# Kernel optimization log

Measured on AMD Instinct MI355X. Metric: run time of the kernel, lower is better.

The kernel has to match this reference:

```python
import jax, jax.numpy as jnp
import numpy as np

N_NODES = 100000


def gcn_conv(x, src, dst, ew, W, b, n):
    """PyG GCNConv: self-loops (weight 1), symmetric norm, linear + bias.
    src/dst/ew already include self-loops."""
    xw = x @ W  # [N, out]
    deg = jax.ops.segment_sum(ew, dst, num_segments=n)  # in-degree with weights
    dinv = jnp.where(deg > 0, jax.lax.rsqrt(deg), 0.0)
    norm = dinv[src] * ew * dinv[dst]  # [E]
    msgs = xw[src] * norm[:, None]  # gather + scale
    out = jax.ops.segment_sum(msgs, dst, num_segments=n)  # scatter-add
    return out + b


def setup_inputs() -> dict:
    key = jax.random.key(0)
    k1, k2, k3, k4, k5 = jax.random.split(key, 5)
    x = jax.random.normal(k1, (N_NODES, 512), dtype=jnp.float32)
    edge_index = jax.random.randint(k2, (2, 3200000), 0, N_NODES, dtype=jnp.int64)
    edge_weight = jax.random.uniform(k3, (3200000,), dtype=jnp.float32)
    W1 = jax.random.normal(k4, (512, 64), dtype=jnp.float32) * (1.0 / np.sqrt(512))
    b1 = jnp.zeros((64,), dtype=jnp.float32)
    W2 = jax.random.normal(k5, (64, 20), dtype=jnp.float32) * (1.0 / np.sqrt(64))
    b2 = jnp.zeros((20,), dtype=jnp.float32)
    return {"x": x, "edge_index": edge_index, "edge_weight": edge_weight,
            "W1": W1, "b1": b1, "W2": W2, "b2": b2}


def reference(x, edge_index, edge_weight, W1, b1, W2, b2):
    n = x.shape[0]
    loops = jnp.arange(n, dtype=edge_index.dtype)
    src = jnp.concatenate([edge_index[0], loops])
    dst = jnp.concatenate([edge_index[1], loops])
    ew = jnp.concatenate([edge_weight, jnp.ones((n,), dtype=edge_weight.dtype)])
    h = gcn_conv(x, src, dst, ew, W1, b1, n)
    h = jax.nn.relu(h)  # dropout is identity in eval mode
    h = gcn_conv(h, src, dst, ew, W2, b2, n)
    return jax.nn.softmax(h, axis=-1)
```

## Files before the change

### kernel.cpp

```cpp
#include <hip/hip_runtime.h>
#include <hip/hip_fp16.h>
#include <math.h>

#define FIN 512
#define H   64
#define C   20
#define CP  32

typedef _Float16 half8 __attribute__((ext_vector_type(8)));
typedef float floatx4 __attribute__((ext_vector_type(4)));

__device__ __forceinline__ int detect_m64(const int* __restrict__ ei) {
    int nz = 0;
    #pragma unroll
    for (int i = 0; i < 32; i++) nz |= ei[2 * i + 1];
    return nz == 0;
}

__device__ __forceinline__ int edge_val(const int* __restrict__ ei, long long idx, int m64) {
    return m64 ? ei[2 * idx] : ei[(int)idx];
}

__global__ void init_kernel(const float* __restrict__ W, _Float16* __restrict__ W1T,
                            unsigned long long* __restrict__ packed, int N) {
    int tid = blockIdx.x * 256 + threadIdx.x;
    if (tid < H * FIN) {
        int n = tid >> 9, k = tid & 511;
        W1T[tid] = (_Float16)W[k * H + n];
    }
    if (tid < N) packed[tid] = 0ULL;
}

#define FIXSCALE 268435456.0f
#define KC 64
#define GM 64
#define HE 2048
__global__ __launch_bounds__(256, 8) void fused_gemm1_hist_kernel(
        const float* __restrict__ x, const _Float16* __restrict__ W1T,
        float* __restrict__ xw1f, int N,
        const int* __restrict__ ei, const float* __restrict__ ew,
        unsigned long long* __restrict__ packed, int* __restrict__ rankdst,
        int E, int GB, int HB) {
    __shared__ _Float16 xsh[GM][72];
    __shared__ _Float16 wsh[64][72];

    int nb = blockIdx.x;
    int minB = (GB < HB) ? GB : HB;
    int isHist, roleId;
    if (nb < 2 * minB) { isHist = !(nb & 1); roleId = nb >> 1; }
    else { int r = nb - 2 * minB; isHist = (HB > GB); roleId = minB + r; }

    if (isHist) {
        int m64 = detect_m64(ei);
        long long base = (long long)roleId * HE + threadIdx.x;
        int d[8]; float w[8];
        #pragma unroll
        for (int u = 0; u < 8; u++) {
            long long e = base + u * 256;
            if (e < E) { d[u] = edge_val(ei, (long long)E + e, m64); w[u] = ew[e]; }
            else d[u] = -1;
        }
        unsigned long long old[8];
        #pragma unroll
        for (int u = 0; u < 8; u++)
            if (d[u] >= 0) {
                unsigned long long add = (1ULL << 40) |
                    (unsigned long long)(w[u] * FIXSCALE + 0.5f);
                old[u] = atomicAdd(&packed[d[u]], add);
            }
        #pragma unroll
        for (int u = 0; u < 8; u++)
            if (d[u] >= 0)
                rankdst[base + u * 256] = ((int)(old[u] >> 40) << 17) | d[u];
        return;
    }

    int tid  = threadIdx.x;
    int wave = tid >> 6;
    int lane = tid & 63;
    int quad = lane >> 4;
    int l16  = lane & 15;
    int row0 = roleId * GM;

    floatx4 acc[4];
    #pragma unroll
    for (int ct = 0; ct < 4; ct++) acc[ct] = (floatx4){0.f, 0.f, 0.f, 0.f};

    int col4  = (tid & 15) * 4;
    int rbase = tid >> 4;
    int wn = tid >> 2;
    int wk = (tid & 3) * 16;

    for (int k0 = 0; k0 < FIN; k0 += KC) {
        #pragma unroll
        for (int it = 0; it < 4; it++) {
            int row = rbase + it * 16;
            int grow = row0 + row; if (grow >= N) grow = N - 1;
            float4 v = *(const float4*)&x[(long long)grow * FIN + k0 + col4];
            _Float16* p = &xsh[row][col4];
            p[0] = (_Float16)v.x; p[1] = (_Float16)v.y;
            p[2] = (_Float16)v.z; p[3] = (_Float16)v.w;
        }
        *(half8*)&wsh[wn][wk]     = *(const half8*)&W1T[wn * FIN + k0 + wk];
        *(half8*)&wsh[wn][wk + 8] = *(const half8*)&W1T[wn * FIN + k0 + wk + 8];
        __syncthreads();
        #pragma unroll
        for (int kk = 0; kk < KC; kk += 32) {
            half8 a0 = *(const half8*)&xsh[wave * 16 + l16][kk + quad * 8];
            #pragma unroll
            for (int ct = 0; ct < 4; ct++) {
                half8 b = *(const half8*)&wsh[ct * 16 + l16][kk + quad * 8];
                acc[ct] = __builtin_amdgcn_mfma_f32_16x16x32_f16(a0, b, acc[ct], 0, 0, 0);
            }
        }
        __syncthreads();
    }
    #pragma unroll
    for (int ct = 0; ct < 4; ct++)
        #pragma unroll
        for (int r = 0; r < 4; r++) {
            int grow = row0 + wave * 16 + quad * 4 + r;
            if (grow < N)
                xw1f[(long long)grow * H + ct * 16 + l16] = acc[ct][r];
        }
}

__global__ void block_sums_kernel(const unsigned long long* __restrict__ packed,
                                  int* __restrict__ bsum, int N) {
    __shared__ int lds[256];
    int t = threadIdx.x;
    int base = blockIdx.x * 1024 + t * 4;
    int s = 0;
    #pragma unroll
    for (int k = 0; k < 4; k++) { int i = base + k; if (i < N) s += (int)(packed[i] >> 40); }
    lds[t] = s; __syncthreads();
    for (int off = 128; off > 0; off >>= 1) {
        if (t < off) lds[t] += lds[t + off];
        __syncthreads();
    }
    if (t == 0) bsum[blockIdx.x] = lds[0];
}

__global__ void scan_local_kernel(const unsigned long long* __restrict__ packed,
                                  const int* __restrict__ bsum,
                                  int* __restrict__ rowptr, float* __restrict__ dinv,
                                  int N, int E) {
    __shared__ int lds[256];
    int t = threadIdx.x, bid = blockIdx.x;
    lds[t] = (t < bid) ? bsum[t] : 0;
    __syncthreads();
    for (int off = 128; off > 0; off >>= 1) {
        if (t < off) lds[t] += lds[t + off];
        __syncthreads();
    }
    int bpre = lds[0];
    __syncthreads();

    int base = bid * 1024 + t * 4;
    int c[4]; int s = 0;
    #pragma unroll
    for (int k = 0; k < 4; k++) {
        int i = base + k;
        if (i < N) {
            unsigned long long v = packed[i];
            c[k] = (int)(v >> 40);
            dinv[i] = rsqrtf((float)(v & ((1ULL << 40) - 1)) * (1.0f / FIXSCALE) + 1.0f);
        } else c[k] = 0;
        s += c[k];
    }
    lds[t] = s; __syncthreads();
    for (int off = 1; off < 256; off <<= 1) {
        int add = (t >= off) ? lds[t - off] : 0;
        __syncthreads();
        lds[t] += add;
        __syncthreads();
    }
    int start = bpre + lds[t] - s;
    #pragma unroll
    for (int k = 0; k < 4; k++) {
        int i = base + k;
        if (i < N) { rowptr[i] = start; start += c[k]; }
    }
    if (bid == 0 && t == 0) rowptr[N] = E;
}

__global__ void scale_kernel(const float* __restrict__ xw1f, const float* __restrict__ dinv,
                             _Float16* __restrict__ xws, int N) {
    long long t = (long long)blockIdx.x * 256 + threadIdx.x;
    if (t >= (long long)N * 8) return;
    int i  = (int)(t >> 3);
    int fo = ((int)t & 7) * 8;
    float di = dinv[i];
    const float4* p = (const float4*)&xw1f[(long long)i * H + fo];
    float4 v0 = p[0], v1 = p[1];
    half8 o;
    o[0] = (_Float16)(v0.x * di); o[1] = (_Float16)(v0.y * di);
    o[2] = (_Float16)(v0.z * di); o[3] = (_Float16)(v0.w * di);
    o[4] = (_Float16)(v1.x * di); o[5] = (_Float16)(v1.y * di);
    o[6] = (_Float16)(v1.z * di); o[7] = (_Float16)(v1.w * di);
    *(half8*)&xws[(long long)i * H + fo] = o;
}

__global__ void fill2_kernel(const int* __restrict__ ei, const float* __restrict__ ew,
                             const int* __restrict__ rowptr,
                             const int* __restrict__ rankdst, int2* __restrict__ edata, int E) {
    int m64 = detect_m64(ei);
    long long t = (long long)blockIdx.x * blockDim.x + threadIdx.x;
    long long e0 = 2 * t;
    if (e0 >= E) return;
    int s0, s1;
    if (m64) {
        int4 sp = *(const int4*)&ei[2 * e0];
        s0 = sp.x; s1 = sp.z;
    } else {
        int2 sp = *(const int2*)&ei[e0];
        s0 = sp.x; s1 = sp.y;
    }
    float2 w = *(const float2*)&ew[e0];
    int2  rd = *(const int2*)&rankdst[e0];
    int d0 = rd.x & 131071, rk0 = rd.x >> 17;
    int d1 = rd.y & 131071, rk1 = rd.y >> 17;
    edata[rowptr[d0] + rk0] = make_int2(s0, __float_as_int(w.x));
    if (e0 + 1 < E)
        edata[rowptr[d1] + rk1] = make_int2(s1, __float_as_int(w.y));
}

#define A1_NODES 16
__global__ __launch_bounds__(256) void agg1g2_kernel(
        const int* __restrict__ rowptr, const int2* __restrict__ edata,
        const _Float16* __restrict__ xws, const float* __restrict__ dinv,
        const float* __restrict__ b1, const float* __restrict__ W2,
        __half* __restrict__ zp, int N) {
    __shared__ float hs[A1_NODES][H + 2];
    __shared__ float w2s[H * C];
    for (int t = threadIdx.x; t < H * C; t += 256) w2s[t] = W2[t];
    __syncthreads();

    const __half* xh = (const __half*)xws;
    int wv = threadIdx.x >> 6;
    int l  = threadIdx.x & 63;
    int g  = l >> 4;
    int q  = l & 15;
    int slot = wv * 4 + g;
    int i  = blockIdx.x * A1_NODES + slot;
    if (i < N) {
        int start = rowptr[i], end = rowptr[i + 1];
        float a0 = 0.f, a1 = 0.f, a2 = 0.f, a3 = 0.f;
        int j = start;
        for (; j + 7 < end; j += 8) {
            int2 e0 = edata[j],     e1 = edata[j + 1], e2 = edata[j + 2], e3 = edata[j + 3];
            int2 e4 = edata[j + 4], e5 = edata[j + 5], e6 = edata[j + 6], e7 = edata[j + 7];
            uint2 u0 = *(const uint2*)&xh[(long long)e0.x * H + 4 * q];
            uint2 u1 = *(const uint2*)&xh[(long long)e1.x * H + 4 * q];
            uint2 u2 = *(const uint2*)&xh[(long long)e2.x * H + 4 * q];
            uint2 u3 = *(const uint2*)&xh[(long long)e3.x * H + 4 * q];
            uint2 u4 = *(const uint2*)&xh[(long long)e4.x * H + 4 * q];
            uint2 u5 = *(const uint2*)&xh[(long long)e5.x * H + 4 * q];
            uint2 u6 = *(const uint2*)&xh[(long long)e6.x * H + 4 * q];
            uint2 u7 = *(const uint2*)&xh[(long long)e7.x * H + 4 * q];
            float n0 = __int_as_float(e0.y), n1 = __int_as_float(e1.y);
            float n2 = __int_as_float(e2.y), n3 = __int_as_float(e3.y);
            float n4 = __int_as_float(e4.y), n5 = __int_as_float(e5.y);
            float n6 = __int_as_float(e6.y), n7 = __int_as_float(e7.y);
            float2 p; 
            p = __half22float2(*(const __half2*)&u0.x); a0 = fmaf(p.x, n0, a0); a1 = fmaf(p.y, n0, a1);
            p = __half22float2(*(const __half2*)&u0.y); a2 = fmaf(p.x, n0, a2); a3 = fmaf(p.y, n0, a3);
            p = __half22float2(*(const __half2*)&u1.x); a0 = fmaf(p.x, n1, a0); a1 = fmaf(p.y, n1, a1);
            p = __half22float2(*(const __half2*)&u1.y); a2 = fmaf(p.x, n1, a2); a3 = fmaf(p.y, n1, a3);
            p = __half22float2(*(const __half2*)&u2.x); a0 = fmaf(p.x, n2, a0); a1 = fmaf(p.y, n2, a1);
            p = __half22float2(*(const __half2*)&u2.y); a2 = fmaf(p.x, n2, a2); a3 = fmaf(p.y, n2, a3);
            p = __half22float2(*(const __half2*)&u3.x); a0 = fmaf(p.x, n3, a0); a1 = fmaf(p.y, n3, a1);
            p = __half22float2(*(const __half2*)&u3.y); a2 = fmaf(p.x, n3, a2); a3 = fmaf(p.y, n3, a3);
            p = __half22float2(*(const __half2*)&u4.x); a0 = fmaf(p.x, n4, a0); a1 = fmaf(p.y, n4, a1);
            p = __half22float2(*(const __half2*)&u4.y); a2 = fmaf(p.x, n4, a2); a3 = fmaf(p.y, n4, a3);
            p = __half22float2(*(const __half2*)&u5.x); a0 = fmaf(p.x, n5, a0); a1 = fmaf(p.y, n5, a1);
            p = __half22float2(*(const __half2*)&u5.y); a2 = fmaf(p.x, n5, a2); a3 = fmaf(p.y, n5, a3);
            p = __half22float2(*(const __half2*)&u6.x); a0 = fmaf(p.x, n6, a0); a1 = fmaf(p.y, n6, a1);
            p = __half22float2(*(const __half2*)&u6.y); a2 = fmaf(p.x, n6, a2); a3 = fmaf(p.y, n6, a3);
            p = __half22float2(*(const __half2*)&u7.x); a0 = fmaf(p.x, n7, a0); a1 = fmaf(p.y, n7, a1);
            p = __half22float2(*(const __half2*)&u7.y); a2 = fmaf(p.x, n7, a2); a3 = fmaf(p.y, n7, a3);
        }
        for (; j < end; j++) {
            int2 e0 = edata[j];
            uint2 u0 = *(const uint2*)&xh[(long long)e0.x * H + 4 * q];
            float n0 = __int_as_float(e0.y);
            float2 p;
            p = __half22float2(*(const __half2*)&u0.x); a0 = fmaf(p.x, n0, a0); a1 = fmaf(p.y, n0, a1);
            p = __half22float2(*(const __half2*)&u0.y); a2 = fmaf(p.x, n0, a2); a3 = fmaf(p.y, n0, a3);
        }
        uint2 us = *(const uint2*)&xh[(long long)i * H + 4 * q];
        float2 p;
        p = __half22float2(*(const __half2*)&us.x); a0 += p.x; a1 += p.y;
        p = __half22float2(*(const __half2*)&us.y); a2 += p.x; a3 += p.y;
        float di = dinv[i];
        float4 bb = *(const float4*)&b1[4 * q];
        hs[slot][4 * q]     = fmaxf(fmaf(a0, di, bb.x), 0.f);
        hs[slot][4 * q + 1] = fmaxf(fmaf(a1, di, bb.y), 0.f);
        hs[slot][4 * q + 2] = fmaxf(fmaf(a2, di, bb.z), 0.f);
        hs[slot][4 * q + 3] = fmaxf(fmaf(a3, di, bb.w), 0.f);
    }
    #pragma unroll
    for (int pass = 0; pass < 2; pass++) {
        int ns = wv * 4 + pass * 2 + (l >> 5);
        int c  = l & 31;
        int node = blockIdx.x * A1_NODES + ns;
        if (node < N) {
            float v = 0.f;
            if (c < C) {
                float acc = 0.f;
                #pragma unroll
                for (int k = 0; k < H; k++) acc = fmaf(hs[ns][k], w2s[k * C + c], acc);
                v = acc * dinv[node];
            }
            zp[(long long)node * CP + c] = __float2half(v);
        }
    }
}

__global__ void agg2_final_kernel(const int* __restrict__ rowptr, const int2* __restrict__ edata,
                                  const __half* __restrict__ zp, const float* __restrict__ dinv,
                                  const float* __restrict__ b2, float* __restrict__ out, int N) {
    long long gid = (long long)blockIdx.x * blockDim.x + threadIdx.x;
    int wid = (int)(gid >> 6);
    int half = (threadIdx.x & 63) >> 5;
    int l = threadIdx.x & 31;
    int i = wid * 2 + half;
    float acc = 0.f;
    bool active = (i < N) && (l < C);
    if (active) {
        int start = rowptr[i], end = rowptr[i + 1];
        int j = start;
        for (; j + 7 < end; j += 8) {
            int2 e0 = edata[j],     e1 = edata[j + 1], e2 = edata[j + 2], e3 = edata[j + 3];
            int2 e4 = edata[j + 4], e5 = edata[j + 5], e6 = edata[j + 6], e7 = edata[j + 7];
            float v0 = __half2float(zp[(long long)e0.x * CP + l]);
            float v1 = __half2float(zp[(long long)e1.x * CP + l]);
            float v2 = __half2float(zp[(long long)e2.x * CP + l]);
            float v3 = __half2float(zp[(long long)e3.x * CP + l]);
            float v4 = __half2float(zp[(long long)e4.x * CP + l]);
            float v5 = __half2float(zp[(long long)e5.x * CP + l]);
            float v6 = __half2float(zp[(long long)e6.x * CP + l]);
            float v7 = __half2float(zp[(long long)e7.x * CP + l]);
            acc = fmaf(v0, __int_as_float(e0.y), acc);
            acc = fmaf(v1, __int_as_float(e1.y), acc);
            acc = fmaf(v2, __int_as_float(e2.y), acc);
            acc = fmaf(v3, __int_as_float(e3.y), acc);
            acc = fmaf(v4, __int_as_float(e4.y), acc);
            acc = fmaf(v5, __int_as_float(e5.y), acc);
            acc = fmaf(v6, __int_as_float(e6.y), acc);
            acc = fmaf(v7, __int_as_float(e7.y), acc);
        }
        for (; j < end; j++) {
            int2 e = edata[j];
            acc = fmaf(__half2float(zp[(long long)e.x * CP + l]), __int_as_float(e.y), acc);
        }
        acc += __half2float(zp[(long long)i * CP + l]);
        acc = fmaf(acc, dinv[i], b2[l]);
    }
    float v = active ? acc : -1e30f;
    float mx = v;
    #pragma unroll
    for (int off = 16; off >= 1; off >>= 1) mx = fmaxf(mx, __shfl_xor(mx, off, 32));
    float ex = active ? expf(v - mx) : 0.f;
    float sm = ex;
    #pragma unroll
    for (int off = 16; off >= 1; off >>= 1) sm += __shfl_xor(sm, off, 32);
    if (active) out[(long long)i * C + l] = ex / sm;
}

static inline size_t align256(size_t x) { return (x + 255) & ~(size_t)255; }

extern "C" void kernel_launch(void* const* d_in, const int* in_sizes, int n_in,
                              void* d_out, int out_size, void* d_ws, size_t ws_size,
                              hipStream_t stream) {
    const float* x  = (const float*)d_in[0];
    const int*   ei = (const int*)d_in[1];
    const float* ew = (const float*)d_in[2];
    const float* W1 = (const float*)d_in[3];
    const float* b1 = (const float*)d_in[4];
    const float* W2 = (const float*)d_in[5];
    const float* b2 = (const float*)d_in[6];
    float* out = (float*)d_out;

    int N = in_sizes[0] / FIN;
    int E = in_sizes[2];
    int NB = (N + 1023) / 1024;

    char* ws = (char*)d_ws;
    size_t off = 0;
    unsigned long long* packed = (unsigned long long*)(ws + off); off = align256(off + (size_t)N * 8);
    float*    dinv    = (float*)(ws + off);    off = align256(off + (size_t)N * 4);
    int*      bsum    = (int*)(ws + off);      off = align256(off + (size_t)NB * 4);
    int*      rowptr  = (int*)(ws + off);      off = align256(off + (size_t)(N + 1) * 4);
    size_t sharedSz = (size_t)E * 8 > (size_t)N * H * 4 ? (size_t)E * 8 : (size_t)N * H * 4;
    float* xw1f  = (float*)(ws + off);
    int2*  edata = (int2*)(ws + off);          off = align256(off + sharedSz);
    _Float16* W1T     = (_Float16*)(ws + off); off = align256(off + (size_t)H * FIN * 2);
    _Float16* xws     = (_Float16*)(ws + off); off = align256(off + (size_t)N * H * 2);
    int*    rankdst = (int*)(ws + off);
    __half* zp      = (__half*)(ws + off);     off = align256(off + (size_t)E * 4);

    int initBlocks = (max(H * FIN, N) + 255) / 256;
    init_kernel<<<initBlocks, 256, 0, stream>>>(W1, W1T, packed, N);

    int GB = (N + GM - 1) / GM;
    int HB = (E + HE - 1) / HE;
    fused_gemm1_hist_kernel<<<GB + HB, 256, 0, stream>>>(
        x, W1T, xw1f, N, ei, ew, packed, rankdst, E, GB, HB);

    block_sums_kernel<<<NB, 256, 0, stream>>>(packed, bsum, N);
    scan_local_kernel<<<NB, 256, 0, stream>>>(packed, bsum, rowptr, dinv, N, E);

    scale_kernel<<<(int)(((long long)N * 8 + 255) / 256), 256, 0, stream>>>(
        xw1f, dinv, xws, N);

    fill2_kernel<<<(int)(((long long)(E + 1) / 2 + 255) / 256), 256, 0, stream>>>(
        ei, ew, rowptr, rankdst, edata, E);

    agg1g2_kernel<<<(N + A1_NODES - 1) / A1_NODES, 256, 0, stream>>>(
        rowptr, edata, xws, dinv, b1, W2, zp, N);

    int waves2 = (N + 1) / 2;
    agg2_final_kernel<<<(int)(((long long)waves2 * 64 + 255) / 256), 256, 0, stream>>>(
        rowptr, edata, zp, dinv, b2, out, N);
}
```

Before: 617.1 us.

## Fuse scale into scan kernel and widen gather vectors in both aggregations

The per-node dinv scaling and fp16 conversion of xw1f moves into scan_local_kernel, using a shared-memory copy of dinv, which removes one kernel launch. The layer-1 aggregation now gives each node 8 lanes that load 16-byte vectors, so a block covers 32 nodes and the gather issues fewer, wider loads. The layer-2 aggregation packs 4 nodes per wave with half2 loads and float2 stores, and runs the softmax shuffles over 16-lane groups. The risks are that scan_local now does much more work per block over only about 98 blocks, which limits parallelism, and that each lane carries more registers.

```diff
diff --git a/kernel.cpp b/kernel.cpp
--- a/kernel.cpp
+++ b/kernel.cpp
@@ -144,8 +144,10 @@
 __global__ void scan_local_kernel(const unsigned long long* __restrict__ packed,
                                   const int* __restrict__ bsum,
                                   int* __restrict__ rowptr, float* __restrict__ dinv,
+                                  const float* __restrict__ xw1f, _Float16* __restrict__ xws,
                                   int N, int E) {
     __shared__ int lds[256];
+    __shared__ float sdinv[1024];
     int t = threadIdx.x, bid = blockIdx.x;
     lds[t] = (t < bid) ? bsum[t] : 0;
     __syncthreads();
@@ -164,8 +166,10 @@
         if (i < N) {
             unsigned long long v = packed[i];
             c[k] = (int)(v >> 40);
-            dinv[i] = rsqrtf((float)(v & ((1ULL << 40) - 1)) * (1.0f / FIXSCALE) + 1.0f);
-        } else c[k] = 0;
+            float di = rsqrtf((float)(v & ((1ULL << 40) - 1)) * (1.0f / FIXSCALE) + 1.0f);
+            dinv[i] = di;
+            sdinv[t * 4 + k] = di;
+        } else { c[k] = 0; sdinv[t * 4 + k] = 0.f; }
         s += c[k];
     }
     lds[t] = s; __syncthreads();
@@ -182,23 +186,23 @@
         if (i < N) { rowptr[i] = start; start += c[k]; }
     }
     if (bid == 0 && t == 0) rowptr[N] = E;
-}
-
-__global__ void scale_kernel(const float* __restrict__ xw1f, const float* __restrict__ dinv,
-                             _Float16* __restrict__ xws, int N) {
-    long long t = (long long)blockIdx.x * 256 + threadIdx.x;
-    if (t >= (long long)N * 8) return;
-    int i  = (int)(t >> 3);
-    int fo = ((int)t & 7) * 8;
-    float di = dinv[i];
-    const float4* p = (const float4*)&xw1f[(long long)i * H + fo];
-    float4 v0 = p[0], v1 = p[1];
-    half8 o;
-    o[0] = (_Float16)(v0.x * di); o[1] = (_Float16)(v0.y * di);
-    o[2] = (_Float16)(v0.z * di); o[3] = (_Float16)(v0.w * di);
-    o[4] = (_Float16)(v1.x * di); o[5] = (_Float16)(v1.y * di);
-    o[6] = (_Float16)(v1.z * di); o[7] = (_Float16)(v1.w * di);
-    *(half8*)&xws[(long long)i * H + fo] = o;
+    __syncthreads();
+
+    for (int u = t; u < 8192; u += 256) {
+        int row = u >> 3;
+        int gi = bid * 1024 + row;
+        if (gi >= N) break;
+        int fo = (u & 7) * 8;
+        float di = sdinv[row];
+        const float4* p = (const float4*)&xw1f[(long long)gi * H + fo];
+        float4 v0 = p[0], v1 = p[1];
+        half8 o;
+        o[0] = (_Float16)(v0.x * di); o[1] = (_Float16)(v0.y * di);
+        o[2] = (_Float16)(v0.z * di); o[3] = (_Float16)(v0.w * di);
+        o[4] = (_Float16)(v1.x * di); o[5] = (_Float16)(v1.y * di);
+        o[6] = (_Float16)(v1.z * di); o[7] = (_Float16)(v1.w * di);
+        *(half8*)&xws[(long long)gi * H + fo] = o;
+    }
 }
 
 __global__ void fill2_kernel(const int* __restrict__ ei, const float* __restrict__ ew,
@@ -225,7 +229,7 @@
         edata[rowptr[d1] + rk1] = make_int2(s1, __float_as_int(w.y));
 }
 
-#define A1_NODES 16
+#define A1_NODES 32
 __global__ __launch_bounds__(256) void agg1g2_kernel(
         const int* __restrict__ rowptr, const int2* __restrict__ edata,
         const _Float16* __restrict__ xws, const float* __restrict__ dinv,
@@ -239,69 +243,71 @@
     const __half* xh = (const __half*)xws;
     int wv = threadIdx.x >> 6;
     int l  = threadIdx.x & 63;
-    int g  = l >> 4;
-    int q  = l & 15;
-    int slot = wv * 4 + g;
+    int g  = l >> 3;
+    int q  = l & 7;
+    int slot = wv * 8 + g;
     int i  = blockIdx.x * A1_NODES + slot;
     if (i < N) {
         int start = rowptr[i], end = rowptr[i + 1];
-        float a0 = 0.f, a1 = 0.f, a2 = 0.f, a3 = 0.f;
+        float a0=0.f,a1=0.f,a2=0.f,a3=0.f,a4=0.f,a5=0.f,a6=0.f,a7=0.f;
         int j = start;
-        for (; j + 7 < end; j += 8) {
-            int2 e0 = edata[j],     e1 = edata[j + 1], e2 = edata[j + 2], e3 = edata[j + 3];
-            int2 e4 = edata[j + 4], e5 = edata[j + 5], e6 = edata[j + 6], e7 = edata[j + 7];
-            uint2 u0 = *(const uint2*)&xh[(long long)e0.x * H + 4 * q];
-            uint2 u1 = *(const uint2*)&xh[(long long)e1.x * H + 4 * q];
-            uint2 u2 = *(const uint2*)&xh[(long long)e2.x * H + 4 * q];
-            uint2 u3 = *(const uint2*)&xh[(long long)e3.x * H + 4 * q];
-            uint2 u4 = *(const uint2*)&xh[(long long)e4.x * H + 4 * q];
-            uint2 u5 = *(const uint2*)&xh[(long long)e5.x * H + 4 * q];
-            uint2 u6 = *(const uint2*)&xh[(long long)e6.x * H + 4 * q];
-            uint2 u7 = *(const uint2*)&xh[(long long)e7.x * H + 4 * q];
+        for (; j + 3 < end; j += 4) {
+            int2 e0 = edata[j], e1 = edata[j + 1], e2 = edata[j + 2], e3 = edata[j + 3];
+            uint4 u0 = *(const uint4*)&xh[(long long)e0.x * H + 8 * q];
+            uint4 u1 = *(const uint4*)&xh[(long long)e1.x * H + 8 * q];
+            uint4 u2 = *(const uint4*)&xh[(long long)e2.x * H + 8 * q];
+            uint4 u3 = *(const uint4*)&xh[(long long)e3.x * H + 8 * q];
             float n0 = __int_as_float(e0.y), n1 = __int_as_float(e1.y);
             float n2 = __int_as_float(e2.y), n3 = __int_as_float(e3.y);
-            float n4 = __int_as_float(e4.y), n5 = __int_as_float(e5.y);
-            float n6 = __int_as_float(e6.y), n7 = __int_as_float(e7.y);
-            float2 p; 
-            p = __half22float2(*(const __half2*)&u0.x); a0 = fmaf(p.x, n0, a0); a1 = fmaf(p.y, n0, a1);
-            p = __half22float2(*(const __half2*)&u0.y); a2 = fmaf(p.x, n0, a2); a3 = fmaf(p.y, n0, a3);
-            p = __half22float2(*(const __half2*)&u1.x); a0 = fmaf(p.x, n1, a0); a1 = fmaf(p.y, n1, a1);
-            p = __half22float2(*(const __half2*)&u1.y); a2 = fmaf(p.x, n1, a2); a3 = fmaf(p.y, n1, a3);
-            p = __half22float2(*(const __half2*)&u2.x); a0 = fmaf(p.x, n2, a0); a1 = fmaf(p.y, n2, a1);
-            p = __half22float2(*(const __half2*)&u2.y); a2 = fmaf(p.x, n2, a2); a3 = fmaf(p.y, n2, a3);
-            p = __half22float2(*(const __half2*)&u3.x); a0 = fmaf(p.x, n3, a0); a1 = fmaf(p.y, n3, a1);
-            p = __half22float2(*(const __half2*)&u3.y); a2 = fmaf(p.x, n3, a2); a3 = fmaf(p.y, n3, a3);
-            p = __half22float2(*(const __half2*)&u4.x); a0 = fmaf(p.x, n4, a0); a1 = fmaf(p.y, n4, a1);
-            p = __half22float2(*(const __half2*)&u4.y); a2 = fmaf(p.x, n4, a2); a3 = fmaf(p.y, n4, a3);
-            p = __half22float2(*(const __half2*)&u5.x); a0 = fmaf(p.x, n5, a0); a1 = fmaf(p.y, n5, a1);
-            p = __half22float2(*(const __half2*)&u5.y); a2 = fmaf(p.x, n5, a2); a3 = fmaf(p.y, n5, a3);
-            p = __half22float2(*(const __half2*)&u6.x); a0 = fmaf(p.x, n6, a0); a1 = fmaf(p.y, n6, a1);
-            p = __half22float2(*(const __half2*)&u6.y); a2 = fmaf(p.x, n6, a2); a3 = fmaf(p.y, n6, a3);
-            p = __half22float2(*(const __half2*)&u7.x); a0 = fmaf(p.x, n7, a0); a1 = fmaf(p.y, n7, a1);
-            p = __half22float2(*(const __half2*)&u7.y); a2 = fmaf(p.x, n7, a2); a3 = fmaf(p.y, n7, a3);
+            float2 p;
+            p = __half22float2(*(const __half2*)&u0.x); a0=fmaf(p.x,n0,a0); a1=fmaf(p.y,n0,a1);
+            p = __half22float2(*(const __half2*)&u0.y); a2=fmaf(p.x,n0,a2); a3=fmaf(p.y,n0,a3);
+            p = __half22float2(*(const __half2*)&u0.z); a4=fmaf(p.x,n0,a4); a5=fmaf(p.y,n0,a5);
+            p = __half22float2(*(const __half2*)&u0.w); a6=fmaf(p.x,n0,a6); a7=fmaf(p.y,n0,a7);
+            p = __half22float2(*(const __half2*)&u1.x); a0=fmaf(p.x,n1,a0); a1=fmaf(p.y,n1,a1);
+            p = __half22float2(*(const __half2*)&u1.y); a2=fmaf(p.x,n1,a2); a3=fmaf(p.y,n1,a3);
+            p = __half22float2(*(const __half2*)&u1.z); a4=fmaf(p.x,n1,a4); a5=fmaf(p.y,n1,a5);
+            p = __half22float2(*(const __half2*)&u1.w); a6=fmaf(p.x,n1,a6); a7=fmaf(p.y,n1,a7);
+            p = __half22float2(*(const __half2*)&u2.x); a0=fmaf(p.x,n2,a0); a1=fmaf(p.y,n2,a1);
+            p = __half22float2(*(const __half2*)&u2.y); a2=fmaf(p.x,n2,a2); a3=fmaf(p.y,n2,a3);
+            p = __half22float2(*(const __half2*)&u2.z); a4=fmaf(p.x,n2,a4); a5=fmaf(p.y,n2,a5);
+            p = __half22float2(*(const __half2*)&u2.w); a6=fmaf(p.x,n2,a6); a7=fmaf(p.y,n2,a7);
+            p = __half22float2(*(const __half2*)&u3.x); a0=fmaf(p.x,n3,a0); a1=fmaf(p.y,n3,a1);
+            p = __half22float2(*(const __half2*)&u3.y); a2=fmaf(p.x,n3,a2); a3=fmaf(p.y,n3,a3);
+            p = __half22float2(*(const __half2*)&u3.z); a4=fmaf(p.x,n3,a4); a5=fmaf(p.y,n3,a5);
+            p = __half22float2(*(const __half2*)&u3.w); a6=fmaf(p.x,n3,a6); a7=fmaf(p.y,n3,a7);
         }
         for (; j < end; j++) {
             int2 e0 = edata[j];
-            uint2 u0 = *(const uint2*)&xh[(long long)e0.x * H + 4 * q];
+            uint4 u0 = *(const uint4*)&xh[(long long)e0.x * H + 8 * q];
             float n0 = __int_as_float(e0.y);
             float2 p;
-            p = __half22float2(*(const __half2*)&u0.x); a0 = fmaf(p.x, n0, a0); a1 = fmaf(p.y, n0, a1);
-            p = __half22float2(*(const __half2*)&u0.y); a2 = fmaf(p.x, n0, a2); a3 = fmaf(p.y, n0, a3);
-        }
-        uint2 us = *(const uint2*)&xh[(long long)i * H + 4 * q];
+            p = __half22float2(*(const __half2*)&u0.x); a0=fmaf(p.x,n0,a0); a1=fmaf(p.y,n0,a1);
+            p = __half22float2(*(const __half2*)&u0.y); a2=fmaf(p.x,n0,a2); a3=fmaf(p.y,n0,a3);
+            p = __half22float2(*(const __half2*)&u0.z); a4=fmaf(p.x,n0,a4); a5=fmaf(p.y,n0,a5);
+            p = __half22float2(*(const __half2*)&u0.w); a6=fmaf(p.x,n0,a6); a7=fmaf(p.y,n0,a7);
+        }
+        uint4 us = *(const uint4*)&xh[(long long)i * H + 8 * q];
         float2 p;
         p = __half22float2(*(const __half2*)&us.x); a0 += p.x; a1 += p.y;
         p = __half22float2(*(const __half2*)&us.y); a2 += p.x; a3 += p.y;
+        p = __half22float2(*(const __half2*)&us.z); a4 += p.x; a5 += p.y;
+        p = __half22float2(*(const __half2*)&us.w); a6 += p.x; a7 += p.y;
         float di = dinv[i];
-        float4 bb = *(const float4*)&b1[4 * q];
-        hs[slot][4 * q]     = fmaxf(fmaf(a0, di, bb.x), 0.f);
-        hs[slot][4 * q + 1] = fmaxf(fmaf(a1, di, bb.y), 0.f);
-        hs[slot][4 * q + 2] = fmaxf(fmaf(a2, di, bb.z), 0.f);
-        hs[slot][4 * q + 3] = fmaxf(fmaf(a3, di, bb.w), 0.f);
-    }
-    #pragma unroll
-    for (int pass = 0; pass < 2; pass++) {
-        int ns = wv * 4 + pass * 2 + (l >> 5);
+        float4 bb0 = *(const float4*)&b1[8 * q];
+        float4 bb1 = *(const float4*)&b1[8 * q + 4];
+        hs[slot][8 * q]     = fmaxf(fmaf(a0, di, bb0.x), 0.f);
+        hs[slot][8 * q + 1] = fmaxf(fmaf(a1, di, bb0.y), 0.f);
+        hs[slot][8 * q + 2] = fmaxf(fmaf(a2, di, bb0.z), 0.f);
+        hs[slot][8 * q + 3] = fmaxf(fmaf(a3, di, bb0.w), 0.f);
+        hs[slot][8 * q + 4] = fmaxf(fmaf(a4, di, bb1.x), 0.f);
+        hs[slot][8 * q + 5] = fmaxf(fmaf(a5, di, bb1.y), 0.f);
+        hs[slot][8 * q + 6] = fmaxf(fmaf(a6, di, bb1.z), 0.f);
+        hs[slot][8 * q + 7] = fmaxf(fmaf(a7, di, bb1.w), 0.f);
+    }
+    #pragma unroll
+    for (int pass = 0; pass < 4; pass++) {
+        int ns = wv * 8 + pass * 2 + (l >> 5);
         int c  = l & 31;
         int node = blockIdx.x * A1_NODES + ns;
         if (node < N) {
@@ -322,50 +328,71 @@
                                   const float* __restrict__ b2, float* __restrict__ out, int N) {
     long long gid = (long long)blockIdx.x * blockDim.x + threadIdx.x;
     int wid = (int)(gid >> 6);
-    int half = (threadIdx.x & 63) >> 5;
-    int l = threadIdx.x & 31;
-    int i = wid * 2 + half;
-    float acc = 0.f;
-    bool active = (i < N) && (l < C);
-    if (active) {
+    int g = (threadIdx.x & 63) >> 4;
+    int q = threadIdx.x & 15;
+    int i = wid * 4 + g;
+    float a0 = 0.f, a1 = 0.f;
+    if (i < N) {
         int start = rowptr[i], end = rowptr[i + 1];
         int j = start;
         for (; j + 7 < end; j += 8) {
             int2 e0 = edata[j],     e1 = edata[j + 1], e2 = edata[j + 2], e3 = edata[j + 3];
             int2 e4 = edata[j + 4], e5 = edata[j + 5], e6 = edata[j + 6], e7 = edata[j + 7];
-            float v0 = __half2float(zp[(long long)e0.x * CP + l]);
-            float v1 = __half2float(zp[(long long)e1.x * CP + l]);
-            float v2 = __half2float(zp[(long long)e2.x * CP + l]);
-            float v3 = __half2float(zp[(long long)e3.x * CP + l]);
-            float v4 = __half2float(zp[(long long)e4.x * CP + l]);
-            float v5 = __half2float(zp[(long long)e5.x * CP + l]);
-            float v6 = __half2float(zp[(long long)e6.x * CP + l]);
-            float v7 = __half2float(zp[(long long)e7.x * CP + l]);
-            acc = fmaf(v0, __int_as_float(e0.y), acc);
-            acc = fmaf(v1, __int_as_float(e1.y), acc);
-            acc = fmaf(v2, __int_as_float(e2.y), acc);
-            acc = fmaf(v3, __int_as_float(e3.y), acc);
-            acc = fmaf(v4, __int_as_float(e4.y), acc);
-            acc = fmaf(v5, __int_as_float(e5.y), acc);
-            acc = fmaf(v6, __int_as_float(e6.y), acc);
-            acc = fmaf(v7, __int_as_float(e7.y), acc);
+            unsigned u0 = *(const unsigned*)&zp[(long long)e0.x * CP + 2 * q];
+            unsigned u1 = *(const unsigned*)&zp[(long long)e1.x * CP + 2 * q];
+            unsigned u2 = *(const unsigned*)&zp[(long long)e2.x * CP + 2 * q];
+            unsigned u3 = *(const unsigned*)&zp[(long long)e3.x * CP + 2 * q];
+            unsigned u4 = *(const unsigned*)&zp[(long long)e4.x * CP + 2 * q];
+            unsigned u5 = *(const unsigned*)&zp[(long long)e5.x * CP + 2 * q];
+            unsigned u6 = *(const unsigned*)&zp[(long long)e6.x * CP + 2 * q];
+            unsigned u7 = *(const unsigned*)&zp[(long long)e7.x * CP + 2 * q];
+            float2 p;
+            p = __half22float2(*(const __half2*)&u0); float n0 = __int_as_float(e0.y);
+            a0 = fmaf(p.x, n0, a0); a1 = fmaf(p.y, n0, a1);
+            p = __half22float2(*(const __half2*)&u1); float n1 = __int_as_float(e1.y);
+            a0 = fmaf(p.x, n1, a0); a1 = fmaf(p.y, n1, a1);
+            p = __half22float2(*(const __half2*)&u2); float n2 = __int_as_float(e2.y);
+            a0 = fmaf(p.x, n2, a0); a1 = fmaf(p.y, n2, a1);
+            p = __half22float2(*(const __half2*)&u3); float n3 = __int_as_float(e3.y);
+            a0 = fmaf(p.x, n3, a0); a1 = fmaf(p.y, n3, a1);
+            p = __half22float2(*(const __half2*)&u4); float n4 = __int_as_float(e4.y);
+            a0 = fmaf(p.x, n4, a0); a1 = fmaf(p.y, n4, a1);
+            p = __half22float2(*(const __half2*)&u5); float n5 = __int_as_float(e5.y);
+            a0 = fmaf(p.x, n5, a0); a1 = fmaf(p.y, n5, a1);
+            p = __half22float2(*(const __half2*)&u6); float n6 = __int_as_float(e6.y);
+            a0 = fmaf(p.x, n6, a0); a1 = fmaf(p.y, n6, a1);
+            p = __half22float2(*(const __half2*)&u7); float n7 = __int_as_float(e7.y);
+            a0 = fmaf(p.x, n7, a0); a1 = fmaf(p.y, n7, a1);
         }
         for (; j < end; j++) {
             int2 e = edata[j];
-            acc = fmaf(__half2float(zp[(long long)e.x * CP + l]), __int_as_float(e.y), acc);
-        }
-        acc += __half2float(zp[(long long)i * CP + l]);
-        acc = fmaf(acc, dinv[i], b2[l]);
-    }
-    float v = active ? acc : -1e30f;
-    float mx = v;
-    #pragma unroll
-    for (int off = 16; off >= 1; off >>= 1) mx = fmaxf(mx, __shfl_xor(mx, off, 32));
-    float ex = active ? expf(v - mx) : 0.f;
-    float sm = ex;
-    #pragma unroll
-    for (int off = 16; off >= 1; off >>= 1) sm += __shfl_xor(sm, off, 32);
-    if (active) out[(long long)i * C + l] = ex / sm;
+            unsigned u = *(const unsigned*)&zp[(long long)e.x * CP + 2 * q];
+            float2 p = __half22float2(*(const __half2*)&u);
+            float n = __int_as_float(e.y);
+            a0 = fmaf(p.x, n, a0); a1 = fmaf(p.y, n, a1);
+        }
+        unsigned us = *(const unsigned*)&zp[(long long)i * CP + 2 * q];
+        float2 ps = __half22float2(*(const __half2*)&us);
+        a0 += ps.x; a1 += ps.y;
+        float di = dinv[i];
+        float bb0 = (q < 10) ? b2[2 * q] : 0.f;
+        float bb1 = (q < 10) ? b2[2 * q + 1] : 0.f;
+        a0 = fmaf(a0, di, bb0);
+        a1 = fmaf(a1, di, bb1);
+    }
+    bool active = (i < N) && (q < 10);
+    float mx = active ? fmaxf(a0, a1) : -1e30f;
+    #pragma unroll
+    for (int off = 8; off >= 1; off >>= 1) mx = fmaxf(mx, __shfl_xor(mx, off, 16));
+    float ex0 = active ? expf(a0 - mx) : 0.f;
+    float ex1 = active ? expf(a1 - mx) : 0.f;
+    float sm = ex0 + ex1;
+    #pragma unroll
+    for (int off = 8; off >= 1; off >>= 1) sm += __shfl_xor(sm, off, 16);
+    if (active) {
+        float2 o = make_float2(ex0 / sm, ex1 / sm);
+        *(float2*)&out[(long long)i * C + 2 * q] = o;
+    }
 }
 
 static inline size_t align256(size_t x) { return (x + 255) & ~(size_t)255; }
@@ -409,10 +436,7 @@
         x, W1T, xw1f, N, ei, ew, packed, rankdst, E, GB, HB);
 
     block_sums_kernel<<<NB, 256, 0, stream>>>(packed, bsum, N);
-    scan_local_kernel<<<NB, 256, 0, stream>>>(packed, bsum, rowptr, dinv, N, E);
-
-    scale_kernel<<<(int)(((long long)N * 8 + 255) / 256), 256, 0, stream>>>(
-        xw1f, dinv, xws, N);
+    scan_local_kernel<<<NB, 256, 0, stream>>>(packed, bsum, rowptr, dinv, xw1f, xws, N, E);
 
     fill2_kernel<<<(int)(((long long)(E + 1) / 2 + 255) / 256), 256, 0, stream>>>(
         ei, ew, rowptr, rankdst, edata, E);
@@ -420,7 +444,7 @@
     agg1g2_kernel<<<(N + A1_NODES - 1) / A1_NODES, 256, 0, stream>>>(
         rowptr, edata, xws, dinv, b1, W2, zp, N);
 
-    int waves2 = (N + 1) / 2;
+    int waves2 = (N + 3) / 4;
     agg2_final_kernel<<<(int)(((long long)waves2 * 64 + 255) / 256), 256, 0, stream>>>(
         rowptr, edata, zp, dinv, b2, out, N);
 }
```

Result: faster. 602.4 us (-2.4%).
